# Kernel optimization log

Measured on AMD Instinct MI355X. Metric: run time of the kernel, lower is better.

Reference implementation:

```python
import jax, jax.numpy as jnp
import numpy as np

RANK, A1, A2, B1, B2 = 64, 64, 64, 64, 64
N_TOKENS = 8192


def _xavier_uniform(key, shape, fan_in, fan_out, dtype=jnp.float32):
    bound = float(np.sqrt(6.0 / (fan_in + fan_out)))
    return jax.random.uniform(key, shape, dtype, -bound, bound)


def setup_inputs() -> dict:
    key = jax.random.key(0)
    kx, ka, kb, kbias = jax.random.split(key, 4)
    x = jax.random.normal(kx, (N_TOKENS, A1 * B1), dtype=jnp.float32)
    # torch xavier on a 3D tensor (rank, d1, d2): fan_in = d1*d2, fan_out = rank*d2
    a = _xavier_uniform(ka, (RANK, A1, A2), A1 * A2, RANK * A2)
    b = _xavier_uniform(kb, (RANK, B1, B2), B1 * B2, RANK * B2)
    bias = jax.random.normal(kbias, (A2 * B2,), dtype=jnp.float32)
    return {"x": x, "a": a, "b": b, "bias": bias}


def reference(x, a, b, bias):
    r, a1, a2 = a.shape
    _, b1, b2 = b.shape
    # w = sum_r kron(a_r, b_r):  w[i*b1+k, j*b2+l] = sum_r a[r,i,j] * b[r,k,l]
    w = jnp.einsum('rij,rkl->ikjl', a, b).reshape(a1 * b1, a2 * b2)
    out = x @ w  # (N, a2*b2)
    return out + bias[None, :]
```

## Files before the change

### kernel.cpp

```cpp
#include <hip/hip_runtime.h>
#include <hip/hip_bf16.h>


#define M_DIM 8192
#define N_DIM 4096
#define K_DIM 4096
#define KT_COUNT 128

typedef __attribute__((ext_vector_type(8))) short short8;
typedef __attribute__((ext_vector_type(4))) float floatx4;

typedef __attribute__((address_space(1))) void gvoid_t;
typedef __attribute__((address_space(3))) void lvoid_t;

static __device__ __forceinline__ void gl_lds16(const void* g, const void* l) {
  __builtin_amdgcn_global_load_lds((gvoid_t*)(unsigned long long)g,
                                   (lvoid_t*)(unsigned int)(unsigned long long)l,
                                   16, 0, 0);
}

static __device__ __forceinline__ unsigned short f2bf(float f) {
  unsigned int u = __builtin_bit_cast(unsigned int, f);
  u = (u + 0x7fffu + ((u >> 16) & 1u)) >> 16;
  return (unsigned short)u;
}

__global__ __launch_bounds__(256) void pack_x_kernel(
    const float* __restrict__ x, unsigned short* __restrict__ Xp) {
  __shared__ float xs[128 * 33];
  const int kt = blockIdx.x;
  const int M0 = blockIdx.y;
  const int t = threadIdx.x;

  {
    const int row = t >> 1;
    const int half = t & 1;
    const float* src = x + (size_t)(M0 * 128 + row) * K_DIM + kt * 32 + half * 16;
    float v[16];
#pragma unroll
    for (int w = 0; w < 4; ++w) {
      float4 vv = ((const float4*)src)[w];
      v[w * 4 + 0] = vv.x; v[w * 4 + 1] = vv.y;
      v[w * 4 + 2] = vv.z; v[w * 4 + 3] = vv.w;
    }
#pragma unroll
    for (int e = 0; e < 16; ++e) xs[row * 33 + half * 16 + e] = v[e];
  }
  __syncthreads();

  unsigned short* dst = Xp + (size_t)(M0 * KT_COUNT + kt) * 4096;
#pragma unroll
  for (int q = 0; q < 2; ++q) {
    const int p = q * 256 + t;
    const int c = p >> 7, mm = p & 127;
    short8 o;
#pragma unroll
    for (int j = 0; j < 8; ++j) o[j] = (short)f2bf(xs[mm * 33 + c * 8 + j]);
    *(short8*)(dst + p * 8) = o;
  }
}

__global__ __launch_bounds__(256) void build_w_kernel(
    const float* __restrict__ a, const float* __restrict__ b,
    unsigned short* __restrict__ Wp) {
  __shared__ float as_lds[1024];
  const int rg = blockIdx.x;
  const int i = rg >> 2;
  const int j0 = (rg & 3) * 16;
  const int k0 = blockIdx.y * 8;
  const int t = threadIdx.x;

  {
    const int r = t >> 2, jq = t & 3;
    float4 v = ((const float4*)(a + (size_t)r * 4096 + i * 64 + j0))[jq];
    ((float4*)as_lds)[r * 4 + jq] = v;
  }
  __syncthreads();

  const int l = t & 63;
  const int jj = t >> 6;
  float acc[4][8];
#pragma unroll
  for (int jp = 0; jp < 4; ++jp)
#pragma unroll
    for (int kb = 0; kb < 8; ++kb) acc[jp][kb] = 0.f;

  const float* bb = b + k0 * 64 + l;
  for (int r = 0; r < 64; ++r) {
    float4 aj = ((const float4*)as_lds)[r * 4 + jj];
    float bv[8];
#pragma unroll
    for (int kb = 0; kb < 8; ++kb) bv[kb] = bb[(size_t)r * 4096 + kb * 64];
    const float av[4] = {aj.x, aj.y, aj.z, aj.w};
#pragma unroll
    for (int jp = 0; jp < 4; ++jp)
#pragma unroll
      for (int kb = 0; kb < 8; ++kb)
        acc[jp][kb] = fmaf(av[jp], bv[kb], acc[jp][kb]);
  }

  const int kt = (i * 64 + k0) >> 5;
  const int c = (k0 & 31) >> 3;
#pragma unroll
  for (int jp = 0; jp < 4; ++jp) {
    const int j = j0 + jj * 4 + jp;
    const int n = j * 64 + l;
    const int blob = (n >> 7) * KT_COUNT + kt;
    const int pos = c * 128 + (n & 127);
    short8 o;
#pragma unroll
    for (int kb = 0; kb < 8; ++kb) o[kb] = (short)f2bf(acc[jp][kb]);
    *(short8*)(Wp + (size_t)blob * 4096 + pos * 8) = o;
  }
}

__global__ __launch_bounds__(256) void gemm_kernel(
    const unsigned short* __restrict__ Xp, const unsigned short* __restrict__ Wp,
    const float* __restrict__ bias, float* __restrict__ out) {
  __shared__ short8 As[512];
  __shared__ short8 Bs[512];

  const int N0 = blockIdx.x;
  const int M0 = blockIdx.y;
  const int t = threadIdx.x;
  const int wave = t >> 6, lane = t & 63;
  const int l16 = lane & 15, quad = lane >> 4;
  const int wm = wave & 1, wn = wave >> 1;

  floatx4 acc[4][4];
#pragma unroll
  for (int mt = 0; mt < 4; ++mt)
#pragma unroll
    for (int nt = 0; nt < 4; ++nt) acc[mt][nt] = (floatx4){0.f, 0.f, 0.f, 0.f};

  const unsigned short* pa = Xp + (size_t)M0 * KT_COUNT * 4096 + (size_t)t * 8;
  const unsigned short* pb = Wp + (size_t)N0 * KT_COUNT * 4096 + (size_t)t * 8;
  const short8* lA0 = As + wave * 64;
  const short8* lA1 = As + 256 + wave * 64;
  const short8* lB0 = Bs + wave * 64;
  const short8* lB1 = Bs + 256 + wave * 64;

  for (int kt = 0; kt < KT_COUNT; ++kt) {
    __syncthreads();
    gl_lds16(pa, lA0);
    gl_lds16(pa + 2048, lA1);
    gl_lds16(pb, lB0);
    gl_lds16(pb + 2048, lB1);
    pa += 4096;
    pb += 4096;
    __syncthreads();

    short8 af[4], bf[4];
#pragma unroll
    for (int mt = 0; mt < 4; ++mt)
      af[mt] = As[quad * 128 + wm * 64 + mt * 16 + l16];
#pragma unroll
    for (int nt = 0; nt < 4; ++nt)
      bf[nt] = Bs[quad * 128 + wn * 64 + nt * 16 + l16];
#pragma unroll
    for (int mt = 0; mt < 4; ++mt)
#pragma unroll
      for (int nt = 0; nt < 4; ++nt)
        acc[mt][nt] = __builtin_amdgcn_mfma_f32_16x16x32_bf16(
            af[mt], bf[nt], acc[mt][nt], 0, 0, 0);
  }

  const int col_base = N0 * 128 + wn * 64;
  const int row_base = M0 * 128 + wm * 64;
#pragma unroll
  for (int nt = 0; nt < 4; ++nt) {
    const int col = col_base + nt * 16 + l16;
    const float bv = bias[col];
#pragma unroll
    for (int mt = 0; mt < 4; ++mt) {
      floatx4 v = acc[mt][nt];
#pragma unroll
      for (int r4 = 0; r4 < 4; ++r4) {
        const int row = row_base + mt * 16 + quad * 4 + r4;
        out[(size_t)row * N_DIM + col] = v[r4] + bv;
      }
    }
  }
}

extern "C" void kernel_launch(void* const* d_in, const int* in_sizes, int n_in,
                              void* d_out, int out_size, void* d_ws, size_t ws_size,
                              hipStream_t stream) {
  const float* x = (const float*)d_in[0];
  const float* a = (const float*)d_in[1];
  const float* b = (const float*)d_in[2];
  const float* bias = (const float*)d_in[3];
  float* out = (float*)d_out;

  unsigned short* Xp = (unsigned short*)d_ws;
  unsigned short* Wp = Xp + (size_t)M_DIM * K_DIM;

  pack_x_kernel<<<dim3(KT_COUNT, M_DIM / 128), 256, 0, stream>>>(x, Xp);
  build_w_kernel<<<dim3(256, 8), 256, 0, stream>>>(a, b, Wp);
  gemm_kernel<<<dim3(N_DIM / 128, M_DIM / 128), 256, 0, stream>>>(Xp, Wp, bias, out);
}
```

Baseline: 568.5 us.

## Merge prep kernels and remap GEMM blocks per XCD for L2 reuse

Folds the x-packing and W-building kernels into one launch that dispatches on block index, removing one kernel launch and letting the two independent prep jobs run concurrently. The GEMM grid becomes 1D and is remapped so that blocks landing on the same XCD (round-robin by block id & 7) share a group of four N tiles, aiming to raise L2 hit rates for the packed W operand. It also adds a partial unroll on the W-build reduction loop. A possible downside is that each XCD now streams all of X, and the merged kernel uses the larger LDS allocation for both paths.

```diff
diff --git a/kernel.cpp b/kernel.cpp
--- a/kernel.cpp
+++ b/kernel.cpp
@@ -25,92 +25,94 @@
   return (unsigned short)u;
 }
 
-__global__ __launch_bounds__(256) void pack_x_kernel(
-    const float* __restrict__ x, unsigned short* __restrict__ Xp) {
-  __shared__ float xs[128 * 33];
-  const int kt = blockIdx.x;
-  const int M0 = blockIdx.y;
+__global__ __launch_bounds__(256) void prep_kernel(
+    const float* __restrict__ x, const float* __restrict__ a,
+    const float* __restrict__ b, unsigned short* __restrict__ Xp,
+    unsigned short* __restrict__ Wp) {
+  __shared__ float lds[128 * 33];
+  const int bid = blockIdx.x;
   const int t = threadIdx.x;
 
-  {
-    const int row = t >> 1;
-    const int half = t & 1;
-    const float* src = x + (size_t)(M0 * 128 + row) * K_DIM + kt * 32 + half * 16;
-    float v[16];
-#pragma unroll
-    for (int w = 0; w < 4; ++w) {
-      float4 vv = ((const float4*)src)[w];
-      v[w * 4 + 0] = vv.x; v[w * 4 + 1] = vv.y;
-      v[w * 4 + 2] = vv.z; v[w * 4 + 3] = vv.w;
-    }
-#pragma unroll
-    for (int e = 0; e < 16; ++e) xs[row * 33 + half * 16 + e] = v[e];
-  }
-  __syncthreads();
-
-  unsigned short* dst = Xp + (size_t)(M0 * KT_COUNT + kt) * 4096;
-#pragma unroll
-  for (int q = 0; q < 2; ++q) {
-    const int p = q * 256 + t;
-    const int c = p >> 7, mm = p & 127;
-    short8 o;
-#pragma unroll
-    for (int j = 0; j < 8; ++j) o[j] = (short)f2bf(xs[mm * 33 + c * 8 + j]);
-    *(short8*)(dst + p * 8) = o;
-  }
-}
-
-__global__ __launch_bounds__(256) void build_w_kernel(
-    const float* __restrict__ a, const float* __restrict__ b,
-    unsigned short* __restrict__ Wp) {
-  __shared__ float as_lds[1024];
-  const int rg = blockIdx.x;
-  const int i = rg >> 2;
-  const int j0 = (rg & 3) * 16;
-  const int k0 = blockIdx.y * 8;
-  const int t = threadIdx.x;
-
-  {
-    const int r = t >> 2, jq = t & 3;
-    float4 v = ((const float4*)(a + (size_t)r * 4096 + i * 64 + j0))[jq];
-    ((float4*)as_lds)[r * 4 + jq] = v;
-  }
-  __syncthreads();
-
-  const int l = t & 63;
-  const int jj = t >> 6;
-  float acc[4][8];
-#pragma unroll
-  for (int jp = 0; jp < 4; ++jp)
-#pragma unroll
-    for (int kb = 0; kb < 8; ++kb) acc[jp][kb] = 0.f;
-
-  const float* bb = b + k0 * 64 + l;
-  for (int r = 0; r < 64; ++r) {
-    float4 aj = ((const float4*)as_lds)[r * 4 + jj];
-    float bv[8];
-#pragma unroll
-    for (int kb = 0; kb < 8; ++kb) bv[kb] = bb[(size_t)r * 4096 + kb * 64];
-    const float av[4] = {aj.x, aj.y, aj.z, aj.w};
+  if (bid < 2048) {
+    const int rg = bid & 255;
+    const int i = rg >> 2;
+    const int j0 = (rg & 3) * 16;
+    const int k0 = (bid >> 8) * 8;
+
+    {
+      const int r = t >> 2, jq = t & 3;
+      float4 v = ((const float4*)(a + (size_t)r * 4096 + i * 64 + j0))[jq];
+      ((float4*)lds)[r * 4 + jq] = v;
+    }
+    __syncthreads();
+
+    const int l = t & 63;
+    const int jj = t >> 6;
+    float acc[4][8];
 #pragma unroll
     for (int jp = 0; jp < 4; ++jp)
 #pragma unroll
-      for (int kb = 0; kb < 8; ++kb)
-        acc[jp][kb] = fmaf(av[jp], bv[kb], acc[jp][kb]);
-  }
-
-  const int kt = (i * 64 + k0) >> 5;
-  const int c = (k0 & 31) >> 3;
-#pragma unroll
-  for (int jp = 0; jp < 4; ++jp) {
-    const int j = j0 + jj * 4 + jp;
-    const int n = j * 64 + l;
-    const int blob = (n >> 7) * KT_COUNT + kt;
-    const int pos = c * 128 + (n & 127);
-    short8 o;
-#pragma unroll
-    for (int kb = 0; kb < 8; ++kb) o[kb] = (short)f2bf(acc[jp][kb]);
-    *(short8*)(Wp + (size_t)blob * 4096 + pos * 8) = o;
+      for (int kb = 0; kb < 8; ++kb) acc[jp][kb] = 0.f;
+
+    const float* bb = b + k0 * 64 + l;
+#pragma unroll 4
+    for (int r = 0; r < 64; ++r) {
+      float4 aj = ((const float4*)lds)[r * 4 + jj];
+      float bv[8];
+#pragma unroll
+      for (int kb = 0; kb < 8; ++kb) bv[kb] = bb[(size_t)r * 4096 + kb * 64];
+      const float av[4] = {aj.x, aj.y, aj.z, aj.w};
+#pragma unroll
+      for (int jp = 0; jp < 4; ++jp)
+#pragma unroll
+        for (int kb = 0; kb < 8; ++kb)
+          acc[jp][kb] = fmaf(av[jp], bv[kb], acc[jp][kb]);
+    }
+
+    const int kt = (i * 64 + k0) >> 5;
+    const int c = (k0 & 31) >> 3;
+#pragma unroll
+    for (int jp = 0; jp < 4; ++jp) {
+      const int j = j0 + jj * 4 + jp;
+      const int n = j * 64 + l;
+      const int blob = (n >> 7) * KT_COUNT + kt;
+      const int pos = c * 128 + (n & 127);
+      short8 o;
+#pragma unroll
+      for (int kb = 0; kb < 8; ++kb) o[kb] = (short)f2bf(acc[jp][kb]);
+      *(short8*)(Wp + (size_t)blob * 4096 + pos * 8) = o;
+    }
+  } else {
+    const int pid = bid - 2048;
+    const int kt = pid & 127;
+    const int M0 = pid >> 7;
+
+    {
+      const int row = t >> 1;
+      const int half = t & 1;
+      const float* src = x + (size_t)(M0 * 128 + row) * K_DIM + kt * 32 + half * 16;
+      float v[16];
+#pragma unroll
+      for (int w = 0; w < 4; ++w) {
+        float4 vv = ((const float4*)src)[w];
+        v[w * 4 + 0] = vv.x; v[w * 4 + 1] = vv.y;
+        v[w * 4 + 2] = vv.z; v[w * 4 + 3] = vv.w;
+      }
+#pragma unroll
+      for (int e = 0; e < 16; ++e) lds[row * 33 + half * 16 + e] = v[e];
+    }
+    __syncthreads();
+
+    unsigned short* dst = Xp + (size_t)(M0 * KT_COUNT + kt) * 4096;
+#pragma unroll
+    for (int q = 0; q < 2; ++q) {
+      const int p = q * 256 + t;
+      const int c = p >> 7, mm = p & 127;
+      short8 o;
+#pragma unroll
+      for (int j = 0; j < 8; ++j) o[j] = (short)f2bf(lds[mm * 33 + c * 8 + j]);
+      *(short8*)(dst + p * 8) = o;
+    }
   }
 }
 
@@ -120,8 +122,12 @@
   __shared__ short8 As[512];
   __shared__ short8 Bs[512];
 
-  const int N0 = blockIdx.x;
-  const int M0 = blockIdx.y;
+  const int bid = blockIdx.x;
+  const int xcd = bid & 7;
+  const int pos = bid >> 3;
+  const int N0 = xcd * 4 + (pos & 3);
+  const int M0 = pos >> 2;
+
   const int t = threadIdx.x;
   const int wave = t >> 6, lane = t & 63;
   const int l16 = lane & 15, quad = lane >> 4;
@@ -195,7 +201,6 @@
   unsigned short* Xp = (unsigned short*)d_ws;
   unsigned short* Wp = Xp + (size_t)M_DIM * K_DIM;
 
-  pack_x_kernel<<<dim3(KT_COUNT, M_DIM / 128), 256, 0, stream>>>(x, Xp);
-  build_w_kernel<<<dim3(256, 8), 256, 0, stream>>>(a, b, Wp);
-  gemm_kernel<<<dim3(N_DIM / 128, M_DIM / 128), 256, 0, stream>>>(Xp, Wp, bias, out);
-}
+  prep_kernel<<<2048 + 8192, 256, 0, stream>>>(x, a, b, Xp, Wp);
+  gemm_kernel<<<2048, 256, 0, stream>>>(Xp, Wp, bias, out);
+}
```

After: 505.9 us. 1.12x faster.
